# Optimization experiments

Hardware: AMD Instinct MI355X
Metric: run time of the kernel (lower is better)

Reference implementation:

```python
import jax, jax.numpy as jnp
import numpy as np

D_IN, D_HID, D_OUT, N_EXP, N_TOK = 1024, 4096, 1024, 8, 4096


def setup_inputs() -> dict:
    key = jax.random.key(0)
    ks = jax.random.split(key, 7)
    x = jax.random.normal(ks[0], (N_TOK, D_IN), dtype=jnp.float32)
    s1 = 1.0 / np.sqrt(D_IN).astype(np.float32)
    s2 = 1.0 / np.sqrt(D_HID).astype(np.float32)
    W1 = jax.random.uniform(ks[1], (N_EXP, D_IN, D_HID), jnp.float32, -s1, s1)
    b1 = jax.random.uniform(ks[2], (N_EXP, D_HID), jnp.float32, -s1, s1)
    W2 = jax.random.uniform(ks[3], (N_EXP, D_HID, D_OUT), jnp.float32, -s2, s2)
    b2 = jax.random.uniform(ks[4], (N_EXP, D_OUT), jnp.float32, -s2, s2)
    Wg = jax.random.uniform(ks[5], (D_IN, N_EXP), jnp.float32, -s1, s1)
    bg = jax.random.uniform(ks[6], (N_EXP,), jnp.float32, -s1, s1)
    return {"x": x, "W1": W1, "b1": b1, "W2": W2, "b2": b2,
            "Wg": Wg, "bg": bg, "top_k": 2}


def reference(x, W1, b1, W2, b2, Wg, bg, top_k):
    # Gating: softmax over experts, then top-k and renormalizing softmax.
    gates = jax.nn.softmax(x @ Wg + bg, axis=-1)            # [N, E]
    topk_vals, topk_idx = jax.lax.top_k(gates, top_k)       # [N, k]
    topk_w = jax.nn.softmax(topk_vals, axis=-1)             # [N, k]
    # Dense all-expert MLP (vectorized replacement for per-token Python loop).
    h = jax.nn.relu(jnp.einsum('nd,edh->neh', x, W1) + b1)  # [N, E, H]
    y = jnp.einsum('neh,eho->neo', h, W2) + b2              # [N, E, O]
    # Combine: gather each token's top-k expert outputs, weighted sum.
    sel = jnp.take_along_axis(y, topk_idx[:, :, None], axis=1)  # [N, k, O]
    out = jnp.sum(topk_w[:, :, None] * sel, axis=1)             # [N, O]
    return out
```

## Files before the change

kernel.cpp:

```cpp
#include <hip/hip_runtime.h>
#include <hip/hip_bf16.h>

#define NTOK 4096
#define DIN  1024
#define DHID 4096
#define DOUT 1024
#define NEXP 8
#define TMAX 72
#define G1BLK (TMAX * (DHID / 128))
#define G2BLK (TMAX * (DOUT / 128))

typedef __hip_bfloat16 bf16;
typedef short short8 __attribute__((ext_vector_type(8)));
typedef short short4v __attribute__((ext_vector_type(4)));
typedef float floatx4 __attribute__((ext_vector_type(4)));

#define WAIT_VM0 0x0F70
#define WAIT_VM4 0x0F74

#define WS_XB    0ull
#define WS_W1T   8388608ull
#define WS_W2T   75497472ull
#define WS_H     142606336ull
#define WS_META  209715200ull
#define MO_CNT    0
#define MO_OFF    64
#define MO_TILE_E 128
#define MO_TILE_S 512
#define MO_TILE_R 896
#define MO_NT     1280
#define MO_CURG   1344
#define MO_T2I    1536
#define MO_T2W    34304
#define MO_ROWS   67072
#define MO_ROWW   99840

__device__ __forceinline__ void gload16(const bf16* g, bf16* l) {
  __builtin_amdgcn_global_load_lds(
      (const __attribute__((address_space(1))) void*)g,
      (__attribute__((address_space(3))) void*)l, 16, 0, 0);
}

__device__ __forceinline__ void transpose_tile(const float* __restrict__ in,
                                               bf16* __restrict__ out,
                                               int R, int C, int cx, int ry,
                                               int e, float* t) {
  size_t ebase = (size_t)e * R * C;
  int c0 = cx * 64, r0 = ry * 64;
  int tid = threadIdx.x;
  int rr = tid >> 4;
  int cq = (tid & 15) * 4;
  #pragma unroll
  for (int i = 0; i < 4; i++) {
    int r = rr + i * 16;
    float4 v = *(const float4*)(in + ebase + (size_t)(r0 + r) * C + c0 + cq);
    t[(cq + 0) * 65 + r] = v.x; t[(cq + 1) * 65 + r] = v.y;
    t[(cq + 2) * 65 + r] = v.z; t[(cq + 3) * 65 + r] = v.w;
  }
  __syncthreads();
  int cc = tid >> 3;
  int rq = (tid & 7) * 8;
  #pragma unroll
  for (int i = 0; i < 2; i++) {
    int c = cc + i * 32;
    union { int4 v; bf16 h[8]; } u;
    #pragma unroll
    for (int j = 0; j < 8; j++) u.h[j] = __float2bfloat16(t[c * 65 + rq + j]);
    *(int4*)(out + ebase + (size_t)(c0 + c) * R + r0 + rq) = u.v;
  }
}

__device__ __forceinline__ void gate_body(const float* __restrict__ x,
                                          const float* __restrict__ Wg,
                                          const float* __restrict__ bg,
                                          bf16* __restrict__ xb,
                                          int* __restrict__ t2i,
                                          float* __restrict__ t2w,
                                          int* __restrict__ cnt, int blk) {
  int wave = threadIdx.x >> 6, lane = threadIdx.x & 63;
  int t = blk * 4 + wave;
  const float* xr = x + (size_t)t * DIN;
  bf16* xbr = xb + (size_t)t * DIN;
  float acc[8] = {0.f, 0.f, 0.f, 0.f, 0.f, 0.f, 0.f, 0.f};
  #pragma unroll
  for (int i = 0; i < 4; i++) {
    int d0 = (lane + i * 64) * 4;
    float4 v = *(const float4*)(xr + d0);
    union { short4v s; bf16 h[4]; } u;
    u.h[0] = __float2bfloat16(v.x); u.h[1] = __float2bfloat16(v.y);
    u.h[2] = __float2bfloat16(v.z); u.h[3] = __float2bfloat16(v.w);
    *(short4v*)(xbr + d0) = u.s;
    float xv4[4] = {v.x, v.y, v.z, v.w};
    #pragma unroll
    for (int c = 0; c < 4; c++) {
      const float* wr = Wg + (size_t)(d0 + c) * 8;
      float4 w0 = *(const float4*)wr;
      float4 w1 = *(const float4*)(wr + 4);
      float xv = xv4[c];
      acc[0] += xv * w0.x; acc[1] += xv * w0.y; acc[2] += xv * w0.z; acc[3] += xv * w0.w;
      acc[4] += xv * w1.x; acc[5] += xv * w1.y; acc[6] += xv * w1.z; acc[7] += xv * w1.w;
    }
  }
  #pragma unroll
  for (int off = 32; off; off >>= 1) {
    #pragma unroll
    for (int e = 0; e < 8; e++) acc[e] += __shfl_xor(acc[e], off, 64);
  }
  if (lane == 0) {
    float p[8], m = -1e30f, s = 0.f;
    #pragma unroll
    for (int e = 0; e < 8; e++) { p[e] = acc[e] + bg[e]; m = fmaxf(m, p[e]); }
    #pragma unroll
    for (int e = 0; e < 8; e++) { p[e] = expf(p[e] - m); s += p[e]; }
    float inv = 1.f / s;
    #pragma unroll
    for (int e = 0; e < 8; e++) p[e] *= inv;
    int i0 = 0;
    #pragma unroll
    for (int e = 1; e < 8; e++) if (p[e] > p[i0]) i0 = e;
    int i1 = (i0 == 0) ? 1 : 0;
    #pragma unroll
    for (int e = 0; e < 8; e++) if (e != i0 && p[e] > p[i1]) i1 = e;
    float d = expf(p[i1] - p[i0]);
    float w0 = 1.f / (1.f + d), w1 = d / (1.f + d);
    t2i[2 * t] = i0; t2i[2 * t + 1] = i1;
    t2w[2 * t] = w0; t2w[2 * t + 1] = w1;
    atomicAdd(&cnt[i0], 1);
    atomicAdd(&cnt[i1], 1);
  }
}

__global__ __launch_bounds__(256)
void k_gate_w1t(const float* __restrict__ x, const float* __restrict__ Wg,
                const float* __restrict__ bg, bf16* __restrict__ xb,
                int* __restrict__ t2i, float* __restrict__ t2w,
                int* __restrict__ cnt,
                const float* __restrict__ W1, bf16* __restrict__ w1t) {
  __shared__ __align__(16) float tsm[64 * 65];
  int b = blockIdx.x;
  if (b < NTOK / 4) {
    gate_body(x, Wg, bg, xb, t2i, t2w, cnt, b);
  } else {
    int tb = b - NTOK / 4;
    int e = tb >> 10;
    int rem = tb & 1023;
    int cx = rem & 63;
    int ry = rem >> 6;
    transpose_tile(W1, w1t, DIN, DHID, cx, ry, e, tsm);
  }
}

__global__ void k_meta(const int* __restrict__ cnt, int* __restrict__ off,
                       int* __restrict__ tile_e, int* __restrict__ tile_s,
                       int* __restrict__ tile_r, int* __restrict__ nt,
                       int* __restrict__ cur_g) {
  int t = threadIdx.x;
  int c[8], o[8], tb[8];
  int acc = 0, tacc = 0;
  #pragma unroll
  for (int e = 0; e < 8; e++) {
    c[e] = cnt[e]; o[e] = acc; acc += c[e];
    tb[e] = tacc; tacc += (c[e] + 127) >> 7;
  }
  if (t < 8) { off[t] = o[t]; cur_g[t] = o[t]; }
  if (t == 0) *nt = tacc;
  if (t < tacc) {
    int e = 0;
    #pragma unroll
    for (int k = 1; k < 8; k++) if (t >= tb[k]) e = k;
    int r = (t - tb[e]) << 7;
    tile_e[t] = e; tile_s[t] = o[e] + r; tile_r[t] = min(128, c[e] - r);
  }
}

__global__ void k_scatter(const int* __restrict__ t2i, const float* __restrict__ t2w,
                          int* __restrict__ cur_g, int* __restrict__ rows,
                          float* __restrict__ roww) {
  __shared__ int lcnt[8], lbase[8];
  if (threadIdx.x < 8) lcnt[threadIdx.x] = 0;
  __syncthreads();
  int t = blockIdx.x * 256 + threadIdx.x;
  int e0 = t2i[2 * t], e1 = t2i[2 * t + 1];
  int p0 = atomicAdd(&lcnt[e0], 1);
  int p1 = atomicAdd(&lcnt[e1], 1);
  __syncthreads();
  if (threadIdx.x < 8)
    lbase[threadIdx.x] = atomicAdd(&cur_g[threadIdx.x], lcnt[threadIdx.x]);
  __syncthreads();
  int a0 = lbase[e0] + p0, a1 = lbase[e1] + p1;
  rows[a0] = t; roww[a0] = t2w[2 * t];
  rows[a1] = t; roww[a1] = t2w[2 * t + 1];
}

template <int MODE>
__device__ __forceinline__ void gemm_tile(
    const bf16* __restrict__ A, const bf16* __restrict__ Bt,
    const float* __restrict__ bias,
    const int* __restrict__ tile_e, const int* __restrict__ tile_s,
    const int* __restrict__ tile_r, const int* __restrict__ nt,
    const int* __restrict__ rows, const float* __restrict__ roww,
    bf16* __restrict__ hout, float* __restrict__ out,
    int K, int N, int hwid, bf16* Al, bf16* Bl) {
  int xcd = hwid & 7, pos = hwid >> 3;
  int tile = xcd * 9 + pos % 9;
  if (tile >= *nt) return;
  int n0 = (pos / 9) * 128;
  int e = tile_e[tile], start = tile_s[tile], mrows = tile_r[tile];
  int tid = threadIdx.x, lane = tid & 63, wave = tid >> 6;
  int wm = wave & 1, wn = wave >> 1;

  int srow = tid >> 2;
  int rot = (srow >> 1) & 3;
  int kc8 = (((tid & 3) - rot) & 3) * 8;
  int ra0 = srow, ra1 = 64 + srow;
  int er0 = ra0 < mrows ? ra0 : 0;
  int er1 = ra1 < mrows ? ra1 : 0;
  size_t ga0, ga1;
  if (MODE == 1) {
    ga0 = (size_t)rows[start + er0] * K;
    ga1 = (size_t)rows[start + er1] * K;
  } else {
    ga0 = (size_t)(start + er0) * K;
    ga1 = (size_t)(start + er1) * K;
  }
  const bf16* ap0 = A + ga0 + kc8;
  const bf16* ap1 = A + ga1 + kc8;
  const bf16* bb = Bt + (size_t)e * K * N + (size_t)n0 * K;
  const bf16* bp0 = bb + (size_t)srow * K + kc8;
  const bf16* bp1 = bb + (size_t)(64 + srow) * K + kc8;

  floatx4 zz = {0.f, 0.f, 0.f, 0.f};
  floatx4 acc[4][4];
  #pragma unroll
  for (int i = 0; i < 4; i++)
    #pragma unroll
    for (int j = 0; j < 4; j++) acc[i][j] = zz;

  int fr = lane & 15;
  int ko = (((lane >> 4) + ((fr >> 1) & 3)) & 3) * 8;

  auto STAGE = [&](int buf, int kk) {
    gload16(ap0 + kk, Al + buf * 4096 + tid * 8);
    gload16(ap1 + kk, Al + buf * 4096 + 2048 + tid * 8);
    gload16(bp0 + kk, Bl + buf * 4096 + tid * 8);
    gload16(bp1 + kk, Bl + buf * 4096 + 2048 + tid * 8);
  };

  STAGE(0, 0);
  STAGE(1, 32);

  int nk = K >> 5;
  int cur = 0;
  for (int t = 0; t < nk; ++t) {
    if (t + 1 < nk) __builtin_amdgcn_s_waitcnt(WAIT_VM4);
    else            __builtin_amdgcn_s_waitcnt(WAIT_VM0);
    __builtin_amdgcn_s_barrier();

    short8 af[4], bfr[4];
    #pragma unroll
    for (int i = 0; i < 4; i++)
      af[i] = *(const short8*)&Al[cur * 4096 + (wm * 64 + i * 16 + fr) * 32 + ko];
    #pragma unroll
    for (int j = 0; j < 4; j++)
      bfr[j] = *(const short8*)&Bl[cur * 4096 + (wn * 64 + j * 16 + fr) * 32 + ko];

    if (t + 2 < nk) {
      int nb = cur + 2; if (nb >= 3) nb -= 3;
      STAGE(nb, (t + 2) * 32);
    }

    #pragma unroll
    for (int i = 0; i < 4; i++)
      #pragma unroll
      for (int j = 0; j < 4; j++)
        acc[i][j] = __builtin_amdgcn_mfma_f32_16x16x32_bf16(af[i], bfr[j], acc[i][j], 0, 0, 0);
    cur = (cur + 1 == 3) ? 0 : cur + 1;
  }

  int col_l = lane & 15, quad = lane >> 4;
  if (MODE == 1) {
    #pragma unroll
    for (int i = 0; i < 4; i++) {
      #pragma unroll
      for (int r = 0; r < 4; r++) {
        int row = wm * 64 + i * 16 + quad * 4 + r;
        if (row < mrows) {
          size_t rb = (size_t)(start + row) * N;
          #pragma unroll
          for (int j = 0; j < 4; j++) {
            int col = n0 + wn * 64 + j * 16 + col_l;
            float v = acc[i][j][r] + bias[e * N + col];
            hout[rb + col] = __float2bfloat16(fmaxf(v, 0.f));
          }
        }
      }
    }
  } else {
    #pragma unroll
    for (int i = 0; i < 4; i++) {
      #pragma unroll
      for (int r = 0; r < 4; r++) {
        int row = wm * 64 + i * 16 + quad * 4 + r;
        if (row < mrows) {
          int tok = rows[start + row];
          float w = roww[start + row];
          size_t ob = (size_t)tok * N;
          #pragma unroll
          for (int j = 0; j < 4; j++) {
            int col = n0 + wn * 64 + j * 16 + col_l;
            float v = (acc[i][j][r] + bias[e * N + col]) * w;
            unsafeAtomicAdd(&out[ob + col], v);
          }
        }
      }
    }
  }
}

__global__ __launch_bounds__(256)
void k_gemm1_w2t(const bf16* __restrict__ A, const bf16* __restrict__ Bt,
                 const float* __restrict__ bias,
                 const int* __restrict__ tile_e, const int* __restrict__ tile_s,
                 const int* __restrict__ tile_r, const int* __restrict__ nt,
                 const int* __restrict__ rows, const float* __restrict__ roww,
                 bf16* __restrict__ hout,
                 const float* __restrict__ W2, bf16* __restrict__ w2t) {
  __shared__ __align__(16) char smem[49152];
  int b = blockIdx.x;
  if (b < G1BLK) {
    gemm_tile<1>(A, Bt, bias, tile_e, tile_s, tile_r, nt, rows, roww,
                 hout, nullptr, DIN, DHID, b,
                 (bf16*)smem, (bf16*)(smem + 24576));
  } else {
    int tb = b - G1BLK;
    int e = tb >> 10;
    int rem = tb & 1023;
    int cx = rem & 15;
    int ry = rem >> 4;
    transpose_tile(W2, w2t, DHID, DOUT, cx, ry, e, (float*)smem);
  }
}

__global__ __launch_bounds__(256)
void k_gemm2(const bf16* __restrict__ A, const bf16* __restrict__ Bt,
             const float* __restrict__ bias,
             const int* __restrict__ tile_e, const int* __restrict__ tile_s,
             const int* __restrict__ tile_r, const int* __restrict__ nt,
             const int* __restrict__ rows, const float* __restrict__ roww,
             float* __restrict__ out) {
  __shared__ __align__(16) char smem[49152];
  gemm_tile<2>(A, Bt, nullptr ? nullptr : Bt ? (const float*)Bt : nullptr,
               nullptr, nullptr, nullptr, nullptr, nullptr, nullptr,
               nullptr, nullptr, 0, 0, 0, nullptr, nullptr);
}

extern "C" void kernel_launch(void* const* d_in, const int* in_sizes, int n_in,
                              void* d_out, int out_size, void* d_ws, size_t ws_size,
                              hipStream_t stream);

__global__ __launch_bounds__(256)
void k_gemm2_real(const bf16* __restrict__ A, const bf16* __restrict__ Bt,
                  const float* __restrict__ bias,
                  const int* __restrict__ tile_e, const int* __restrict__ tile_s,
                  const int* __restrict__ tile_r, const int* __restrict__ nt,
                  const int* __restrict__ rows, const float* __restrict__ roww,
                  float* __restrict__ out) {
  __shared__ __align__(16) char smem[49152];
  gemm_tile<2>(A, Bt, bias, tile_e, tile_s, tile_r, nt, rows, roww,
               nullptr, out, DHID, DOUT, (int)blockIdx.x,
               (bf16*)smem, (bf16*)(smem + 24576));
}

extern "C" void kernel_launch(void* const* d_in, const int* in_sizes, int n_in,
                              void* d_out, int out_size, void* d_ws, size_t ws_size,
                              hipStream_t stream) {
  const float* x  = (const float*)d_in[0];
  const float* W1 = (const float*)d_in[1];
  const float* b1 = (const float*)d_in[2];
  const float* W2 = (const float*)d_in[3];
  const float* b2 = (const float*)d_in[4];
  const float* Wg = (const float*)d_in[5];
  const float* bg = (const float*)d_in[6];
  float* out = (float*)d_out;
  char* ws = (char*)d_ws;

  bf16* xb  = (bf16*)(ws + WS_XB);
  bf16* w1t = (bf16*)(ws + WS_W1T);
  bf16* w2t = (bf16*)(ws + WS_W2T);
  bf16* h   = (bf16*)(ws + WS_H);
  char* meta = ws + WS_META;
  int*   cnt    = (int*)(meta + MO_CNT);
  int*   off    = (int*)(meta + MO_OFF);
  int*   tile_e = (int*)(meta + MO_TILE_E);
  int*   tile_s = (int*)(meta + MO_TILE_S);
  int*   tile_r = (int*)(meta + MO_TILE_R);
  int*   nt     = (int*)(meta + MO_NT);
  int*   cur_g  = (int*)(meta + MO_CURG);
  int*   t2i    = (int*)(meta + MO_T2I);
  float* t2w    = (float*)(meta + MO_T2W);
  int*   rows   = (int*)(meta + MO_ROWS);
  float* roww   = (float*)(meta + MO_ROWW);

  hipMemsetAsync(cnt, 0, 64, stream);
  hipMemsetAsync(d_out, 0, (size_t)out_size * sizeof(float), stream);

  k_gate_w1t<<<NTOK / 4 + 8192, 256, 0, stream>>>(x, Wg, bg, xb, t2i, t2w, cnt,
                                                  W1, w1t);
  k_meta<<<1, 128, 0, stream>>>(cnt, off, tile_e, tile_s, tile_r, nt, cur_g);
  k_scatter<<<NTOK / 256, 256, 0, stream>>>(t2i, t2w, cur_g, rows, roww);
  k_gemm1_w2t<<<G1BLK + 8192, 256, 0, stream>>>(xb, w1t, b1, tile_e, tile_s,
                                                tile_r, nt, rows, roww, h,
                                                W2, w2t);
  k_gemm2_real<<<G2BLK, 256, 0, stream>>>(h, w2t, b2, tile_e, tile_s, tile_r,
                                          nt, rows, roww, out);
}
```

Measured before the change: 627.6 us.

## Split-K the second expert GEMM and fold tile metadata into consumers

```diff
diff --git a/kernel.cpp b/kernel.cpp
--- a/kernel.cpp
+++ b/kernel.cpp
@@ -8,7 +8,8 @@
 #define NEXP 8
 #define TMAX 72
 #define G1BLK (TMAX * (DHID / 128))
-#define G2BLK (TMAX * (DOUT / 128))
+#define SPLITK 2
+#define KH (DHID / SPLITK)
 
 typedef __hip_bfloat16 bf16;
 typedef short short8 __attribute__((ext_vector_type(8)));
@@ -24,12 +25,7 @@
 #define WS_H     142606336ull
 #define WS_META  209715200ull
 #define MO_CNT    0
-#define MO_OFF    64
-#define MO_TILE_E 128
-#define MO_TILE_S 512
-#define MO_TILE_R 896
-#define MO_NT     1280
-#define MO_CURG   1344
+#define MO_CURG   32
 #define MO_T2I    1536
 #define MO_T2W    34304
 #define MO_ROWS   67072
@@ -39,6 +35,23 @@
   __builtin_amdgcn_global_load_lds(
       (const __attribute__((address_space(1))) void*)g,
       (__attribute__((address_space(3))) void*)l, 16, 0, 0);
+}
+
+__device__ __forceinline__ int tile_lookup(const int* __restrict__ cnt, int tile,
+                                           int& e, int& start, int& mrows) {
+  int o = 0, tacc = 0;
+  e = -1; start = 0; mrows = 0;
+  #pragma unroll
+  for (int k = 0; k < 8; k++) {
+    int c = cnt[k];
+    int nb = (c + 127) >> 7;
+    if (e < 0 && tile < tacc + nb) {
+      e = k; int r = (tile - tacc) << 7;
+      start = o + r; mrows = min(128, c - r);
+    }
+    tacc += nb; o += c;
+  }
+  return tacc;
 }
 
 __device__ __forceinline__ void transpose_tile(const float* __restrict__ in,
@@ -150,32 +163,9 @@
   }
 }
 
-__global__ void k_meta(const int* __restrict__ cnt, int* __restrict__ off,
-                       int* __restrict__ tile_e, int* __restrict__ tile_s,
-                       int* __restrict__ tile_r, int* __restrict__ nt,
-                       int* __restrict__ cur_g) {
-  int t = threadIdx.x;
-  int c[8], o[8], tb[8];
-  int acc = 0, tacc = 0;
-  #pragma unroll
-  for (int e = 0; e < 8; e++) {
-    c[e] = cnt[e]; o[e] = acc; acc += c[e];
-    tb[e] = tacc; tacc += (c[e] + 127) >> 7;
-  }
-  if (t < 8) { off[t] = o[t]; cur_g[t] = o[t]; }
-  if (t == 0) *nt = tacc;
-  if (t < tacc) {
-    int e = 0;
-    #pragma unroll
-    for (int k = 1; k < 8; k++) if (t >= tb[k]) e = k;
-    int r = (t - tb[e]) << 7;
-    tile_e[t] = e; tile_s[t] = o[e] + r; tile_r[t] = min(128, c[e] - r);
-  }
-}
-
 __global__ void k_scatter(const int* __restrict__ t2i, const float* __restrict__ t2w,
-                          int* __restrict__ cur_g, int* __restrict__ rows,
-                          float* __restrict__ roww) {
+                          const int* __restrict__ cnt, int* __restrict__ cur_g,
+                          int* __restrict__ rows, float* __restrict__ roww) {
   __shared__ int lcnt[8], lbase[8];
   if (threadIdx.x < 8) lcnt[threadIdx.x] = 0;
   __syncthreads();
@@ -184,8 +174,12 @@
   int p0 = atomicAdd(&lcnt[e0], 1);
   int p1 = atomicAdd(&lcnt[e1], 1);
   __syncthreads();
-  if (threadIdx.x < 8)
-    lbase[threadIdx.x] = atomicAdd(&cur_g[threadIdx.x], lcnt[threadIdx.x]);
+  if (threadIdx.x < 8) {
+    int base = atomicAdd(&cur_g[threadIdx.x], lcnt[threadIdx.x]);
+    int off = 0;
+    for (int k = 0; k < threadIdx.x; k++) off += cnt[k];
+    lbase[threadIdx.x] = off + base;
+  }
   __syncthreads();
   int a0 = lbase[e0] + p0, a1 = lbase[e1] + p1;
   rows[a0] = t; roww[a0] = t2w[2 * t];
@@ -195,17 +189,17 @@
 template <int MODE>
 __device__ __forceinline__ void gemm_tile(
     const bf16* __restrict__ A, const bf16* __restrict__ Bt,
-    const float* __restrict__ bias,
-    const int* __restrict__ tile_e, const int* __restrict__ tile_s,
-    const int* __restrict__ tile_r, const int* __restrict__ nt,
+    const float* __restrict__ bias, const int* __restrict__ cnt,
     const int* __restrict__ rows, const float* __restrict__ roww,
     bf16* __restrict__ hout, float* __restrict__ out,
-    int K, int N, int hwid, bf16* Al, bf16* Bl) {
+    int K, int N, int hwid, int kbase, int nk, bool addb,
+    bf16 (&Al)[3][4096], bf16 (&Bl)[3][4096]) {
   int xcd = hwid & 7, pos = hwid >> 3;
   int tile = xcd * 9 + pos % 9;
-  if (tile >= *nt) return;
+  int e, start, mrows;
+  int ntt = tile_lookup(cnt, tile, e, start, mrows);
+  if (tile >= ntt) return;
   int n0 = (pos / 9) * 128;
-  int e = tile_e[tile], start = tile_s[tile], mrows = tile_r[tile];
   int tid = threadIdx.x, lane = tid & 63, wave = tid >> 6;
   int wm = wave & 1, wn = wave >> 1;
 
@@ -223,9 +217,9 @@
     ga0 = (size_t)(start + er0) * K;
     ga1 = (size_t)(start + er1) * K;
   }
-  const bf16* ap0 = A + ga0 + kc8;
-  const bf16* ap1 = A + ga1 + kc8;
-  const bf16* bb = Bt + (size_t)e * K * N + (size_t)n0 * K;
+  const bf16* ap0 = A + ga0 + kbase + kc8;
+  const bf16* ap1 = A + ga1 + kbase + kc8;
+  const bf16* bb = Bt + (size_t)e * K * N + (size_t)n0 * K + kbase;
   const bf16* bp0 = bb + (size_t)srow * K + kc8;
   const bf16* bp1 = bb + (size_t)(64 + srow) * K + kc8;
 
@@ -239,17 +233,17 @@
   int fr = lane & 15;
   int ko = (((lane >> 4) + ((fr >> 1) & 3)) & 3) * 8;
 
-  auto STAGE = [&](int buf, int kk) {
-    gload16(ap0 + kk, Al + buf * 4096 + tid * 8);
-    gload16(ap1 + kk, Al + buf * 4096 + 2048 + tid * 8);
-    gload16(bp0 + kk, Bl + buf * 4096 + tid * 8);
-    gload16(bp1 + kk, Bl + buf * 4096 + 2048 + tid * 8);
-  };
+#define STAGE(buf, kk)                                    \
+  do {                                                    \
+    gload16(ap0 + (kk), &Al[buf][tid * 8]);               \
+    gload16(ap1 + (kk), &Al[buf][2048 + tid * 8]);        \
+    gload16(bp0 + (kk), &Bl[buf][tid * 8]);               \
+    gload16(bp1 + (kk), &Bl[buf][2048 + tid * 8]);        \
+  } while (0)
 
   STAGE(0, 0);
   STAGE(1, 32);
 
-  int nk = K >> 5;
   int cur = 0;
   for (int t = 0; t < nk; ++t) {
     if (t + 1 < nk) __builtin_amdgcn_s_waitcnt(WAIT_VM4);
@@ -259,10 +253,10 @@
     short8 af[4], bfr[4];
     #pragma unroll
     for (int i = 0; i < 4; i++)
-      af[i] = *(const short8*)&Al[cur * 4096 + (wm * 64 + i * 16 + fr) * 32 + ko];
+      af[i] = *(const short8*)&Al[cur][(wm * 64 + i * 16 + fr) * 32 + ko];
     #pragma unroll
     for (int j = 0; j < 4; j++)
-      bfr[j] = *(const short8*)&Bl[cur * 4096 + (wn * 64 + j * 16 + fr) * 32 + ko];
+      bfr[j] = *(const short8*)&Bl[cur][(wn * 64 + j * 16 + fr) * 32 + ko];
 
     if (t + 2 < nk) {
       int nb = cur + 2; if (nb >= 3) nb -= 3;
@@ -276,6 +270,7 @@
         acc[i][j] = __builtin_amdgcn_mfma_f32_16x16x32_bf16(af[i], bfr[j], acc[i][j], 0, 0, 0);
     cur = (cur + 1 == 3) ? 0 : cur + 1;
   }
+#undef STAGE
 
   int col_l = lane & 15, quad = lane >> 4;
   if (MODE == 1) {
@@ -308,7 +303,8 @@
           #pragma unroll
           for (int j = 0; j < 4; j++) {
             int col = n0 + wn * 64 + j * 16 + col_l;
-            float v = (acc[i][j][r] + bias[e * N + col]) * w;
+            float b = addb ? bias[e * N + col] : 0.f;
+            float v = (acc[i][j][r] + b) * w;
             unsafeAtomicAdd(&out[ob + col], v);
           }
         }
@@ -319,18 +315,17 @@
 
 __global__ __launch_bounds__(256)
 void k_gemm1_w2t(const bf16* __restrict__ A, const bf16* __restrict__ Bt,
-                 const float* __restrict__ bias,
-                 const int* __restrict__ tile_e, const int* __restrict__ tile_s,
-                 const int* __restrict__ tile_r, const int* __restrict__ nt,
+                 const float* __restrict__ bias, const int* __restrict__ cnt,
                  const int* __restrict__ rows, const float* __restrict__ roww,
                  bf16* __restrict__ hout,
                  const float* __restrict__ W2, bf16* __restrict__ w2t) {
   __shared__ __align__(16) char smem[49152];
   int b = blockIdx.x;
   if (b < G1BLK) {
-    gemm_tile<1>(A, Bt, bias, tile_e, tile_s, tile_r, nt, rows, roww,
-                 hout, nullptr, DIN, DHID, b,
-                 (bf16*)smem, (bf16*)(smem + 24576));
+    auto& Al = *reinterpret_cast<bf16(*)[3][4096]>((void*)smem);
+    auto& Bl = *reinterpret_cast<bf16(*)[3][4096]>((void*)(smem + 24576));
+    gemm_tile<1>(A, Bt, bias, cnt, rows, roww, hout, nullptr,
+                 DIN, DHID, b, 0, DIN / 32, true, Al, Bl);
   } else {
     int tb = b - G1BLK;
     int e = tb >> 10;
@@ -343,32 +338,15 @@
 
 __global__ __launch_bounds__(256)
 void k_gemm2(const bf16* __restrict__ A, const bf16* __restrict__ Bt,
-             const float* __restrict__ bias,
-             const int* __restrict__ tile_e, const int* __restrict__ tile_s,
-             const int* __restrict__ tile_r, const int* __restrict__ nt,
+             const float* __restrict__ bias, const int* __restrict__ cnt,
              const int* __restrict__ rows, const float* __restrict__ roww,
              float* __restrict__ out) {
-  __shared__ __align__(16) char smem[49152];
-  gemm_tile<2>(A, Bt, nullptr ? nullptr : Bt ? (const float*)Bt : nullptr,
-               nullptr, nullptr, nullptr, nullptr, nullptr, nullptr,
-               nullptr, nullptr, 0, 0, 0, nullptr, nullptr);
-}
-
-extern "C" void kernel_launch(void* const* d_in, const int* in_sizes, int n_in,
-                              void* d_out, int out_size, void* d_ws, size_t ws_size,
-                              hipStream_t stream);
-
-__global__ __launch_bounds__(256)
-void k_gemm2_real(const bf16* __restrict__ A, const bf16* __restrict__ Bt,
-                  const float* __restrict__ bias,
-                  const int* __restrict__ tile_e, const int* __restrict__ tile_s,
-                  const int* __restrict__ tile_r, const int* __restrict__ nt,
-                  const int* __restrict__ rows, const float* __restrict__ roww,
-                  float* __restrict__ out) {
-  __shared__ __align__(16) char smem[49152];
-  gemm_tile<2>(A, Bt, bias, tile_e, tile_s, tile_r, nt, rows, roww,
-               nullptr, out, DHID, DOUT, (int)blockIdx.x,
-               (bf16*)smem, (bf16*)(smem + 24576));
+  __shared__ bf16 Al[3][4096];
+  __shared__ bf16 Bl[3][4096];
+  int hwid = blockIdx.x + blockIdx.y * gridDim.x;
+  gemm_tile<2>(A, Bt, bias, cnt, rows, roww, nullptr, out,
+               DHID, DOUT, hwid, blockIdx.z * KH, KH / 32, blockIdx.z == 0,
+               Al, Bl);
 }
 
 extern "C" void kernel_launch(void* const* d_in, const int* in_sizes, int n_in,
@@ -390,27 +368,20 @@
   bf16* h   = (bf16*)(ws + WS_H);
   char* meta = ws + WS_META;
   int*   cnt    = (int*)(meta + MO_CNT);
-  int*   off    = (int*)(meta + MO_OFF);
-  int*   tile_e = (int*)(meta + MO_TILE_E);
-  int*   tile_s = (int*)(meta + MO_TILE_S);
-  int*   tile_r = (int*)(meta + MO_TILE_R);
-  int*   nt     = (int*)(meta + MO_NT);
   int*   cur_g  = (int*)(meta + MO_CURG);
   int*   t2i    = (int*)(meta + MO_T2I);
   float* t2w    = (float*)(meta + MO_T2W);
   int*   rows   = (int*)(meta + MO_ROWS);
   float* roww   = (float*)(meta + MO_ROWW);
 
-  hipMemsetAsync(cnt, 0, 64, stream);
+  hipMemsetAsync(meta, 0, 64, stream);
   hipMemsetAsync(d_out, 0, (size_t)out_size * sizeof(float), stream);
 
   k_gate_w1t<<<NTOK / 4 + 8192, 256, 0, stream>>>(x, Wg, bg, xb, t2i, t2w, cnt,
                                                   W1, w1t);
-  k_meta<<<1, 128, 0, stream>>>(cnt, off, tile_e, tile_s, tile_r, nt, cur_g);
-  k_scatter<<<NTOK / 256, 256, 0, stream>>>(t2i, t2w, cur_g, rows, roww);
-  k_gemm1_w2t<<<G1BLK + 8192, 256, 0, stream>>>(xb, w1t, b1, tile_e, tile_s,
-                                                tile_r, nt, rows, roww, h,
+  k_scatter<<<NTOK / 256, 256, 0, stream>>>(t2i, t2w, cnt, cur_g, rows, roww);
+  k_gemm1_w2t<<<G1BLK + 8192, 256, 0, stream>>>(xb, w1t, b1, cnt, rows, roww, h,
                                                 W2, w2t);
-  k_gemm2_real<<<G2BLK, 256, 0, stream>>>(h, w2t, b2, tile_e, tile_s, tile_r,
-                                          nt, rows, roww, out);
-}
+  k_gemm2<<<dim3(TMAX, DOUT / 128, SPLITK), 256, 0, stream>>>(
+      h, w2t, b2, cnt, rows, roww, out);
+}
```

Measured after the change: 638.4 us. No clear change (+1.7%).
